# Performance work log

Measured on AMD Instinct MI355X. Metric: run time of the kernel, lower is better.

## Reference

```python
import jax, jax.numpy as jnp
import numpy as np


def _conv3d(x, w):
    # x: [N, C, D, H, W], w: [O, I, K, K, K] -> [N, O, D', H', W'] VALID conv
    return jax.lax.conv_general_dilated(
        x, w, window_strides=(1, 1, 1), padding='VALID',
        dimension_numbers=('NCDHW', 'OIDHW', 'NCDHW'))


def conv4d(x, w):
    # x: [B, C, D1, D2, D3, D4]; w: [O, I, K1, K2, K3, K4]
    # Decompose 4D conv as a sum over K1 taps of 3D convs; the sliced D1
    # window is folded into the batch dimension so XLA's 3D conv does the work.
    B, C, D1, D2, D3, D4 = x.shape
    O, I, K1, K2, K3, K4 = w.shape
    D1o = D1 - K1 + 1
    out = None
    for i in range(K1):  # small fixed loop over kernel taps (K1=3)
        xs = jax.lax.dynamic_slice_in_dim(x, i, D1o, axis=2)      # [B,C,D1o,D2,D3,D4]
        xs = xs.transpose(0, 2, 1, 3, 4, 5).reshape(B * D1o, C, D2, D3, D4)
        y = _conv3d(xs, w[:, :, i])                                # [B*D1o,O,d2,d3,d4]
        out = y if out is None else out + y
    d2, d3, d4 = out.shape[2], out.shape[3], out.shape[4]
    out = out.reshape(B, D1o, O, d2, d3, d4).transpose(0, 2, 1, 3, 4, 5)
    return out  # [B, O, D1o, d2, d3, d4]


def setup_inputs() -> dict:
    key = jax.random.key(0)
    k1, k2 = jax.random.split(key)
    pic_in = jax.random.normal(k1, (2, 16, 8, 8, 64, 64), dtype=jnp.float32)
    # convNd weight: [out_channels, in_channels, K, K, K, K], no bias
    weight = jax.random.normal(k2, (32, 16, 3, 3, 3, 3), dtype=jnp.float32) * 0.05
    return {"pic_in": pic_in, "weight": weight}


def reference(pic_in, weight):
    # ConvKernel.forward: 4D conv (stride 1, padding 0, no bias) + ReLU
    return jax.nn.relu(conv4d(pic_in, weight))
```

## Files before the change

### kernel.cpp

```cpp
#include <hip/hip_runtime.h>


typedef __attribute__((ext_vector_type(8))) __bf16 bf16x8;
typedef __attribute__((ext_vector_type(16))) float f32x16;

#define CSTRIDE 262144

#define WT_OFF 0
#define XB_OFF 131072

__global__ __launch_bounds__(256) void prep(const float* __restrict__ x,
                                            const float* __restrict__ w,
                                            unsigned char* __restrict__ ws) {
  int blk = blockIdx.x;
  if (blk < 512) {
    __bf16* xb = (__bf16*)(ws + XB_OFF);
    int n = blk * 256 + threadIdx.x;
    int cg = n & 15;
    int d3 = (n >> 4) & 63;
    int d2 = (n >> 10) & 7;
    int d1 = (n >> 13) & 7;
    int b = n >> 16;
    const float* gx =
        x + ((((b * 16) * 8 + d1) * 8 + d2) * 64 + d3) * 64 + cg * 4;
    float4 v[16];
#pragma unroll
    for (int c = 0; c < 16; ++c)
      v[c] = *(const float4*)(gx + (size_t)c * CSTRIDE);
    __bf16* row = xb + ((((b * 8 + d1) * 8 + d2) * 64 + d3) * 1024);
#pragma unroll
    for (int ch = 0; ch < 2; ++ch) {
#pragma unroll
      for (int j = 0; j < 4; ++j) {
        bf16x8 o;
#pragma unroll
        for (int cc = 0; cc < 8; ++cc)
          o[cc] = (__bf16)(((const float*)&v[ch * 8 + cc])[j]);
        *(bf16x8*)(row + ch * 512 + (cg * 4 + j) * 8) = o;
      }
    }
  } else {
    int o = blk - 512;
    __bf16* wT = (__bf16*)(ws + WT_OFF);
#pragma unroll
    for (int base = 0; base < 1296; base += 256) {
      int idx = base + threadIdx.x;
      if (idx < 1296) {
        int c = idx / 81, t = idx % 81;
        wT[t * 512 + o * 16 + c] = (__bf16)w[o * 1296 + idx];
      }
    }
  }
}

__global__ __launch_bounds__(256, 2) void conv_mfma(
    const unsigned char* __restrict__ ws, float* __restrict__ out) {
  const unsigned char* wTb = ws + WT_OFF;
  const unsigned char* xbb = ws + XB_OFF;

  int bid = blockIdx.x;
  int g = bid % 72;
  int chunk = bid / 72;
  int b = g / 36;
  int e1 = (g / 6) % 6;
  int e2 = g % 6;
  int r0 = chunk * 8;

  int lane = threadIdx.x & 63;
  int wave = threadIdx.x >> 6;
  int th = wave & 1;
  int rg = wave >> 1;
  int m32 = lane & 31;
  int half = lane >> 5;

  int aoff = half * 1024 + (th * 32 + m32) * 16;
  int woff = m32 * 32 + half * 16;

  const unsigned char* abase0 =
      xbb + (size_t)(((b * 8 + e1) * 8 + e2) * 64 + r0 + rg * 4) * 2048 + aoff;
  const unsigned char* wbase = wTb + woff;

  f32x16 acc[4];
#pragma unroll
  for (int i = 0; i < 4; ++i)
#pragma unroll
    for (int r = 0; r < 16; ++r) acc[i][r] = 0.f;

  bf16x8 ab[2][6];
  bf16x8 bb[2][9];

#pragma unroll
  for (int j = 0; j < 6; ++j)
    ab[0][j] = *(const bf16x8*)(abase0 + j * 2048);
#pragma unroll
  for (int t9 = 0; t9 < 9; ++t9)
    bb[0][t9] = *(const bf16x8*)(wbase + t9 * 1024);

#pragma unroll
  for (int p = 0; p < 9; ++p) {
    const int k1 = p / 3, k2 = p % 3;
    const unsigned char* acur = abase0 + (k1 * 8 + k2) * 131072;
#pragma unroll
    for (int k4 = 0; k4 < 3; ++k4) {
      const int sc = (p * 3 + k4) & 1, sn = sc ^ 1;
      if (k4 < 2) {
#pragma unroll
        for (int j = 0; j < 6; ++j)
          ab[sn][j] = *(const bf16x8*)(acur + j * 2048 + (k4 + 1) * 16);
      } else if (p < 8) {
        const int nk1 = (p + 1) / 3, nk2 = (p + 1) % 3;
        const unsigned char* anxt = abase0 + (nk1 * 8 + nk2) * 131072;
#pragma unroll
        for (int j = 0; j < 6; ++j)
          ab[sn][j] = *(const bf16x8*)(anxt + j * 2048);
#pragma unroll
        for (int t9 = 0; t9 < 9; ++t9)
          bb[(p + 1) & 1][t9] =
              *(const bf16x8*)(wbase + (p + 1) * 9216 + t9 * 1024);
      }
#pragma unroll
      for (int k3 = 0; k3 < 3; ++k3) {
        bf16x8 bf = bb[p & 1][k3 * 3 + k4];
#pragma unroll
        for (int i = 0; i < 4; ++i)
          acc[i] = __builtin_amdgcn_mfma_f32_32x32x16_bf16(ab[sc][i + k3], bf,
                                                           acc[i], 0, 0, 0);
      }
    }
  }

  __shared__ float scr[4][32 * 33];
  float* s = scr[wave];
  int e4 = th * 32 + m32;
  size_t obase = ((((size_t)b * 32) * 6 + e1) * 6 + e2) * 3844;
#pragma unroll
  for (int i = 0; i < 4; ++i) {
    int e3 = r0 + rg * 4 + i;
#pragma unroll
    for (int r = 0; r < 16; ++r) {
      int m = (r & 3) + 8 * (r >> 2) + 4 * half;
      s[m * 33 + m32] = acc[i][r];
    }
    if (e3 < 62) {
#pragma unroll
      for (int it = 0; it < 16; ++it) {
        int o = it * 2 + half;
        float v = fmaxf(s[m32 * 33 + o], 0.f);
        if (e4 < 62)
          out[obase + (size_t)o * 138384 + (size_t)e3 * 62 + e4] = v;
      }
    }
  }
}

extern "C" void kernel_launch(void* const* d_in, const int* in_sizes, int n_in,
                              void* d_out, int out_size, void* d_ws,
                              size_t ws_size, hipStream_t stream) {
  const float* x = (const float*)d_in[0];
  const float* w = (const float*)d_in[1];
  float* out = (float*)d_out;
  unsigned char* ws = (unsigned char*)d_ws;
  prep<<<dim3(544), dim3(256), 0, stream>>>(x, w, ws);
  conv_mfma<<<dim3(8 * 72), dim3(256), 0, stream>>>(ws, out);
}
```

Baseline: 130.3 us.

## Stage input rows into LDS via async global_load_lds with double buffering

```diff
diff --git a/kernel.cpp b/kernel.cpp
--- a/kernel.cpp
+++ b/kernel.cpp
@@ -8,6 +8,19 @@
 
 #define WT_OFF 0
 #define XB_OFF 131072
+
+typedef __attribute__((address_space(1))) const unsigned int gu32;
+typedef __attribute__((address_space(3))) unsigned int lu32;
+
+__device__ __forceinline__ void async_cp16(const void* g, void* l) {
+  __builtin_amdgcn_global_load_lds((gu32*)g, (lu32*)l, 16, 0, 0);
+}
+
+__device__ __forceinline__ void wait_cp_done() {
+  __builtin_amdgcn_sched_barrier(0);
+  asm volatile("s_waitcnt vmcnt(9)");
+  __builtin_amdgcn_sched_barrier(0);
+}
 
 __global__ __launch_bounds__(256) void prep(const float* __restrict__ x,
                                             const float* __restrict__ w,
@@ -58,27 +71,24 @@
   const unsigned char* wTb = ws + WT_OFF;
   const unsigned char* xbb = ws + XB_OFF;
 
+  __shared__ __align__(16) unsigned char lds[4 * 16384 + 64];
+
   int bid = blockIdx.x;
-  int g = bid % 72;
-  int chunk = bid / 72;
+  int chunk = bid & 7;
+  int g = bid >> 3;
   int b = g / 36;
   int e1 = (g / 6) % 6;
   int e2 = g % 6;
-  int r0 = chunk * 8;
 
   int lane = threadIdx.x & 63;
   int wave = threadIdx.x >> 6;
-  int th = wave & 1;
-  int rg = wave >> 1;
   int m32 = lane & 31;
   int half = lane >> 5;
-
-  int aoff = half * 1024 + (th * 32 + m32) * 16;
-  int woff = m32 * 32 + half * 16;
-
-  const unsigned char* abase0 =
-      xbb + (size_t)(((b * 8 + e1) * 8 + e2) * 64 + r0 + rg * 4) * 2048 + aoff;
-  const unsigned char* wbase = wTb + woff;
+  int r0b = chunk * 8 + wave * 2;
+
+  unsigned char* ldsw = lds + wave * 16384;
+  int ab_lane = half * 1024 + m32 * 16;
+  const unsigned char* wbase = wTb + m32 * 32 + half * 16;
 
   f32x16 acc[4];
 #pragma unroll
@@ -86,68 +96,123 @@
 #pragma unroll
     for (int r = 0; r < 16; ++r) acc[i][r] = 0.f;
 
-  bf16x8 ab[2][6];
   bf16x8 bb[2][9];
 
-#pragma unroll
-  for (int j = 0; j < 6; ++j)
-    ab[0][j] = *(const bf16x8*)(abase0 + j * 2048);
+  __builtin_amdgcn_sched_barrier(0);
+  {
+    const unsigned char* base =
+        xbb + (size_t)(((b * 8 + e1) * 8 + e2) * 64) * 2048;
+#pragma unroll
+    for (int j = 0; j < 4; ++j) {
+      int row = r0b + j;
+      if (row > 63) row = 63;
+      const unsigned char* gr = base + (size_t)row * 2048 + lane * 16;
+      async_cp16(gr, ldsw + j * 2048);
+      async_cp16(gr + 1024, ldsw + j * 2048 + 1024);
+    }
+  }
+  __builtin_amdgcn_sched_barrier(0);
 #pragma unroll
   for (int t9 = 0; t9 < 9; ++t9)
     bb[0][t9] = *(const bf16x8*)(wbase + t9 * 1024);
 
 #pragma unroll
   for (int p = 0; p < 9; ++p) {
-    const int k1 = p / 3, k2 = p % 3;
-    const unsigned char* acur = abase0 + (k1 * 8 + k2) * 131072;
-#pragma unroll
-    for (int k4 = 0; k4 < 3; ++k4) {
-      const int sc = (p * 3 + k4) & 1, sn = sc ^ 1;
-      if (k4 < 2) {
-#pragma unroll
-        for (int j = 0; j < 6; ++j)
-          ab[sn][j] = *(const bf16x8*)(acur + j * 2048 + (k4 + 1) * 16);
-      } else if (p < 8) {
-        const int nk1 = (p + 1) / 3, nk2 = (p + 1) % 3;
-        const unsigned char* anxt = abase0 + (nk1 * 8 + nk2) * 131072;
-#pragma unroll
-        for (int j = 0; j < 6; ++j)
-          ab[sn][j] = *(const bf16x8*)(anxt + j * 2048);
-#pragma unroll
-        for (int t9 = 0; t9 < 9; ++t9)
-          bb[(p + 1) & 1][t9] =
-              *(const bf16x8*)(wbase + (p + 1) * 9216 + t9 * 1024);
-      }
-#pragma unroll
-      for (int k3 = 0; k3 < 3; ++k3) {
-        bf16x8 bf = bb[p & 1][k3 * 3 + k4];
-#pragma unroll
-        for (int i = 0; i < 4; ++i)
-          acc[i] = __builtin_amdgcn_mfma_f32_32x32x16_bf16(ab[sc][i + k3], bf,
-                                                           acc[i], 0, 0, 0);
-      }
-    }
-  }
-
-  __shared__ float scr[4][32 * 33];
-  float* s = scr[wave];
-  int e4 = th * 32 + m32;
+    const int cb = p & 1, nb = cb ^ 1;
+    const unsigned char* abase = ldsw + cb * 8192 + ab_lane;
+
+    wait_cp_done();
+
+    bf16x8 a0[8], a1[8], a2[8];
+#pragma unroll
+    for (int j = 0; j < 4; ++j)
+#pragma unroll
+      for (int th = 0; th < 2; ++th)
+        a0[j * 2 + th] = *(const bf16x8*)(abase + j * 2048 + th * 512);
+#pragma unroll
+    for (int k3 = 0; k3 < 3; ++k3)
+#pragma unroll
+      for (int i = 0; i < 2; ++i)
+#pragma unroll
+        for (int th = 0; th < 2; ++th)
+          acc[i * 2 + th] = __builtin_amdgcn_mfma_f32_32x32x16_bf16(
+              a0[(i + k3) * 2 + th], bb[cb][k3 * 3 + 0], acc[i * 2 + th], 0, 0,
+              0);
+#pragma unroll
+    for (int j = 0; j < 4; ++j)
+#pragma unroll
+      for (int th = 0; th < 2; ++th)
+        a1[j * 2 + th] = *(const bf16x8*)(abase + j * 2048 + th * 512 + 16);
+#pragma unroll
+    for (int k3 = 0; k3 < 3; ++k3)
+#pragma unroll
+      for (int i = 0; i < 2; ++i)
+#pragma unroll
+        for (int th = 0; th < 2; ++th)
+          acc[i * 2 + th] = __builtin_amdgcn_mfma_f32_32x32x16_bf16(
+              a1[(i + k3) * 2 + th], bb[cb][k3 * 3 + 1], acc[i * 2 + th], 0, 0,
+              0);
+#pragma unroll
+    for (int j = 0; j < 4; ++j)
+#pragma unroll
+      for (int th = 0; th < 2; ++th)
+        a2[j * 2 + th] = *(const bf16x8*)(abase + j * 2048 + th * 512 + 32);
+
+    __builtin_amdgcn_sched_barrier(0);
+    if (p < 8) {
+      const int np = p + 1;
+      const int nk1 = np / 3, nk2 = np - nk1 * 3;
+      const unsigned char* base =
+          xbb + (size_t)(((b * 8 + e1 + nk1) * 8 + (e2 + nk2)) * 64) * 2048;
+      unsigned char* dst = ldsw + nb * 8192;
+#pragma unroll
+      for (int j = 0; j < 4; ++j) {
+        int row = r0b + j;
+        if (row > 63) row = 63;
+        const unsigned char* gr = base + (size_t)row * 2048 + lane * 16;
+        async_cp16(gr, dst + j * 2048);
+        async_cp16(gr + 1024, dst + j * 2048 + 1024);
+      }
+    }
+    __builtin_amdgcn_sched_barrier(0);
+    if (p < 8) {
+#pragma unroll
+      for (int t9 = 0; t9 < 9; ++t9)
+        bb[nb][t9] = *(const bf16x8*)(wbase + (p + 1) * 9216 + t9 * 1024);
+    }
+    __builtin_amdgcn_sched_barrier(0);
+#pragma unroll
+    for (int k3 = 0; k3 < 3; ++k3)
+#pragma unroll
+      for (int i = 0; i < 2; ++i)
+#pragma unroll
+        for (int th = 0; th < 2; ++th)
+          acc[i * 2 + th] = __builtin_amdgcn_mfma_f32_32x32x16_bf16(
+              a2[(i + k3) * 2 + th], bb[cb][k3 * 3 + 2], acc[i * 2 + th], 0, 0,
+              0);
+  }
+
+  float* sc = (float*)(void*)ldsw;
   size_t obase = ((((size_t)b * 32) * 6 + e1) * 6 + e2) * 3844;
 #pragma unroll
-  for (int i = 0; i < 4; ++i) {
-    int e3 = r0 + rg * 4 + i;
-#pragma unroll
-    for (int r = 0; r < 16; ++r) {
-      int m = (r & 3) + 8 * (r >> 2) + 4 * half;
-      s[m * 33 + m32] = acc[i][r];
-    }
-    if (e3 < 62) {
-#pragma unroll
-      for (int it = 0; it < 16; ++it) {
-        int o = it * 2 + half;
-        float v = fmaxf(s[m32 * 33 + o], 0.f);
-        if (e4 < 62)
-          out[obase + (size_t)o * 138384 + (size_t)e3 * 62 + e4] = v;
+  for (int i = 0; i < 2; ++i) {
+    int e3 = r0b + i;
+#pragma unroll
+    for (int th = 0; th < 2; ++th) {
+#pragma unroll
+      for (int r = 0; r < 16; ++r) {
+        int m = (r & 3) + 8 * (r >> 2) + 4 * half;
+        sc[m * 33 + m32] = acc[i * 2 + th][r];
+      }
+      int e4 = th * 32 + m32;
+      if (e3 < 62) {
+#pragma unroll
+        for (int it = 0; it < 16; ++it) {
+          int o = it * 2 + half;
+          float v = fmaxf(sc[m32 * 33 + o], 0.f);
+          if (e4 < 62)
+            out[obase + (size_t)o * 138384 + (size_t)e3 * 62 + e4] = v;
+        }
       }
     }
   }
@@ -161,5 +226,5 @@
   float* out = (float*)d_out;
   unsigned char* ws = (unsigned char*)d_ws;
   prep<<<dim3(544), dim3(256), 0, stream>>>(x, w, ws);
-  conv_mfma<<<dim3(8 * 72), dim3(256), 0, stream>>>(ws, out);
-}
+  conv_mfma<<<dim3(576), dim3(256), 0, stream>>>(ws, out);
+}
```

Result: faster. 117.5 us (-9.8%).
